# Kernel tuning notes

Measured on AMD Instinct MI355X. Metric: run time of the kernel, lower is better.

## Reference

```python
import jax, jax.numpy as jnp
import numpy as np

B, T, IN, H, L = 256, 80, 39, 256, 5


def _xavier(key, shape):
    fan_out, fan_in = shape[0], shape[1]
    std = (2.0 / (fan_in + fan_out)) ** 0.5
    return std * jax.random.normal(key, shape, dtype=jnp.float32)


def setup_inputs() -> dict:
    key = jax.random.key(0)
    ks = jax.random.split(key, 4 + 2 * L)
    x = jax.random.normal(ks[0], (B, T, IN), dtype=jnp.float32)
    # PyTorch LSTM params, gate order (i, f, g, o); biases zero per init.
    W_ih0 = _xavier(ks[1], (4 * H, IN))                       # layer 0 input weights
    W_ih_rest = jnp.stack([_xavier(ks[2 + l], (4 * H, H)) for l in range(L - 1)])  # [L-1,4H,H]
    W_hh = jnp.stack([_xavier(ks[1 + L + l], (4 * H, H)) for l in range(L)])       # [L,4H,H]
    b_ih = jnp.zeros((L, 4 * H), dtype=jnp.float32)
    b_hh = jnp.zeros((L, 4 * H), dtype=jnp.float32)
    fc_w = _xavier(ks[2 * L + 1], (1, H))
    fc_b = jnp.zeros((1,), dtype=jnp.float32)
    return {"x": x, "W_ih0": W_ih0, "W_ih_rest": W_ih_rest, "W_hh": W_hh,
            "b_ih": b_ih, "b_hh": b_hh, "fc_w": fc_w, "fc_b": fc_b}


def _lstm_layer(xs, W_ih, W_hh_l, b_ih_l, b_hh_l):
    # xs: [B,T,D]. Precompute input projection for all timesteps (one big GEMM).
    x_proj = jnp.einsum('btd,gd->btg', xs, W_ih) + b_ih_l + b_hh_l  # [B,T,4H]

    def step(carry, xp):
        h, c = carry
        gates = xp + h @ W_hh_l.T                 # [B,4H]
        i, f, g, o = jnp.split(gates, 4, axis=-1)
        c = jax.nn.sigmoid(f) * c + jax.nn.sigmoid(i) * jnp.tanh(g)
        h = jax.nn.sigmoid(o) * jnp.tanh(c)
        return (h, c), h

    b = xs.shape[0]
    h0 = jnp.zeros((b, H), dtype=xs.dtype)
    _, hs = jax.lax.scan(step, (h0, h0), jnp.swapaxes(x_proj, 0, 1))
    return jnp.swapaxes(hs, 0, 1)  # [B,T,H]


def reference(x, W_ih0, W_ih_rest, W_hh, b_ih, b_hh, fc_w, fc_b):
    h = _lstm_layer(x, W_ih0, W_hh[0], b_ih[0], b_hh[0])
    for l in range(1, L):
        h = _lstm_layer(h, W_ih_rest[l - 1], W_hh[l], b_ih[l], b_hh[l])
    out = jnp.einsum('bth,oh->bto', h, fc_w) + fc_b  # [B,T,1]
    return out[..., 0]  # [B,T]
```

## Files before the change

kernel.cpp:

```cpp
#include <hip/hip_runtime.h>

#define B_ 256
#define T_ 80
#define IN_ 39
#define H_ 256
#define G_ 1024
#define L_ 5
#define TC_ 16
#define NCH_ 5

#define XP_FLOATS   (B_ * TC_ * G_)
#define HBUF_FLOATS (B_ * T_ * H_)
#define CBUF_FLOATS (B_ * H_)
#define WG_FLOATS   (L_ * G_ * H_)
#define HX_FLOATS   (2 * 32 * 2048)
#define FLG_OFF_FLOATS (XP_FLOATS + HBUF_FLOATS + CBUF_FLOATS + WG_FLOATS + HX_FLOATS)

#define AG __HIP_MEMORY_SCOPE_AGENT

__device__ __forceinline__ float sigm(float x) { return 1.0f / (1.0f + expf(-x)); }
__device__ __forceinline__ void fma4(float4& a, float s, const float4& w) {
    a.x = fmaf(s, w.x, a.x); a.y = fmaf(s, w.y, a.y);
    a.z = fmaf(s, w.z, a.z); a.w = fmaf(s, w.w, a.w);
}
__device__ __forceinline__ void red4(float4& a) {
    a.x += __shfl_xor(a.x, 32); a.y += __shfl_xor(a.y, 32);
    a.z += __shfl_xor(a.z, 32); a.w += __shfl_xor(a.w, 32);
}

__device__ __forceinline__ void ld_mall_32B(const float* p, float4& a, float4& b) {
    asm volatile("global_load_dwordx4 %0, %2, off sc0 sc1\n\t"
                 "global_load_dwordx4 %1, %2, off offset:16 sc0 sc1\n\t"
                 "s_waitcnt vmcnt(0)"
                 : "=&v"(a), "=&v"(b) : "v"(p) : "memory");
}

extern "C" __global__ void __launch_bounds__(256)
wt_kernel(const float* __restrict__ Whh, float* __restrict__ Wg) {
    const int gid = blockIdx.x * 256 + threadIdx.x;
    const int g4 = gid & 3;
    const int j  = (gid >> 2) & 31;
    const int k  = (gid >> 7) & 255;
    const int s  = (gid >> 15) & 7;
    const int l  = gid >> 18;
    Wg[gid] = Whh[((size_t)(l * 1024 + g4 * 256 + s * 32 + j)) * 256 + k];
}

extern "C" __global__ void __launch_bounds__(256)
proj_kernel(const float* __restrict__ src, const float* __restrict__ Wih,
            const float* __restrict__ bihl, const float* __restrict__ bhhl,
            float* __restrict__ xp, int K, int t0) {
    __shared__ float As[16 * 68];
    __shared__ float Bs[16 * 68];
    const int tid = threadIdx.x;
    const int mt = blockIdx.x >> 4, nt = blockIdx.x & 15;
    const int tx = tid & 15, ty = tid >> 4;
    const int lr = tid >> 2, lc4 = (tid & 3) << 2;

    const int ar = mt * 64 + lr;
    const int ab = ar >> 4;
    const int at = t0 + (ar & 15);
    const float* arow = src + ((size_t)ab * T_ + at) * K;
    const int brow_idx = (lr & 3) * 256 + nt * 16 + (lr >> 2);
    const float* brow = Wih + (size_t)brow_idx * K;

    float acc[4][4];
    #pragma unroll
    for (int i = 0; i < 4; ++i)
        #pragma unroll
        for (int j = 0; j < 4; ++j) acc[i][j] = 0.0f;

    for (int k0 = 0; k0 < K; k0 += 16) {
        __syncthreads();
        if (K == IN_) {
            #pragma unroll
            for (int i = 0; i < 4; ++i) {
                int k = k0 + lc4 + i;
                As[(lc4 + i) * 68 + lr] = (k < IN_) ? arow[k] : 0.0f;
                Bs[(lc4 + i) * 68 + lr] = (k < IN_) ? brow[k] : 0.0f;
            }
        } else {
            float4 av = *(const float4*)(arow + k0 + lc4);
            float4 bv = *(const float4*)(brow + k0 + lc4);
            As[(lc4 + 0) * 68 + lr] = av.x;
            As[(lc4 + 1) * 68 + lr] = av.y;
            As[(lc4 + 2) * 68 + lr] = av.z;
            As[(lc4 + 3) * 68 + lr] = av.w;
            Bs[(lc4 + 0) * 68 + lr] = bv.x;
            Bs[(lc4 + 1) * 68 + lr] = bv.y;
            Bs[(lc4 + 2) * 68 + lr] = bv.z;
            Bs[(lc4 + 3) * 68 + lr] = bv.w;
        }
        __syncthreads();
        #pragma unroll
        for (int kk = 0; kk < 16; ++kk) {
            float4 a4 = *(const float4*)&As[kk * 68 + ty * 4];
            float4 b4 = *(const float4*)&Bs[kk * 68 + tx * 4];
            acc[0][0] += a4.x * b4.x; acc[0][1] += a4.x * b4.y;
            acc[0][2] += a4.x * b4.z; acc[0][3] += a4.x * b4.w;
            acc[1][0] += a4.y * b4.x; acc[1][1] += a4.y * b4.y;
            acc[1][2] += a4.y * b4.z; acc[1][3] += a4.y * b4.w;
            acc[2][0] += a4.z * b4.x; acc[2][1] += a4.z * b4.y;
            acc[2][2] += a4.z * b4.z; acc[2][3] += a4.z * b4.w;
            acc[3][0] += a4.w * b4.x; acc[3][1] += a4.w * b4.y;
            acc[3][2] += a4.w * b4.z; acc[3][3] += a4.w * b4.w;
        }
    }
    const int unit = nt * 16 + tx;
    const float bs0 = bihl[0 * 256 + unit] + bhhl[0 * 256 + unit];
    const float bs1 = bihl[1 * 256 + unit] + bhhl[1 * 256 + unit];
    const float bs2 = bihl[2 * 256 + unit] + bhhl[2 * 256 + unit];
    const float bs3 = bihl[3 * 256 + unit] + bhhl[3 * 256 + unit];
    #pragma unroll
    for (int i = 0; i < 4; ++i) {
        const int row = mt * 64 + ty * 4 + i;
        float4 o;
        o.x = acc[i][0] + bs0; o.y = acc[i][1] + bs1;
        o.z = acc[i][2] + bs2; o.w = acc[i][3] + bs3;
        *(float4*)&xp[(size_t)row * G_ + unit * 4] = o;
    }
}

extern "C" __global__ void __launch_bounds__(512, 2)
rec8_kernel(const float* __restrict__ xp, const float* __restrict__ Wg_l,
            float* __restrict__ hbuf, float* __restrict__ cbuf,
            float* __restrict__ hx, int* __restrict__ flg,
            int t0, int chkb, int first) {
    __shared__ float sH[2048];
    __shared__ float sP[8 * 32 * 36];

    const int tid = threadIdx.x;
    const int bid = blockIdx.x;
    const int grp = bid & 31;
    const int s   = bid >> 5;
    const int jj  = tid & 31;
    const int ks  = tid >> 5;
    const int w   = tid >> 6;
    const int fb  = (tid >> 5) & 7;
    const int fj  = tid & 31;
    const int bglob = grp * 8 + fb;
    const int unit  = s * 32 + fj;
    int* flg_g = flg + grp * 32;

    const float4* Wg4 = (const float4*)Wg_l + (size_t)s * 8192;
    float4 wreg[16];
    #pragma unroll
    for (int kk = 0; kk < 16; ++kk)
        wreg[kk] = Wg4[(size_t)(ks * 16 + kk) * 32 + jj];

    float creg = 0.0f;
    if (tid < 256 && !first) creg = cbuf[(size_t)bglob * H_ + unit];

    const float4* sH4 = (const float4*)sH;

    for (int tt = 0; tt < TC_; ++tt) {
        const int t = t0 + tt;

        float x0 = 0.f, x1 = 0.f, x2 = 0.f, x3 = 0.f;
        if (tid < 256) {
            const float4 xv = *(const float4*)&xp[((size_t)bglob * TC_ + tt) * G_ + unit * 4];
            x0 = xv.x; x1 = xv.y; x2 = xv.z; x3 = xv.w;
        }

        if (tt == 0) {
            if (first) {
                for (int i = tid; i < 2048; i += 512) sH[i] = 0.0f;
            } else if (tid < 256) {
                const int u = tid;
                #pragma unroll
                for (int bb = 0; bb < 8; ++bb)
                    sH[u * 8 + bb] = hbuf[((size_t)(grp * 8 + bb) * T_ + (t0 - 1)) * H_ + u];
            }
        } else {
            if (tid < 8) {
                const int tgt = chkb + tt;
                while (__hip_atomic_load(flg_g + tid, __ATOMIC_RELAXED, AG) < tgt)
                    __builtin_amdgcn_s_sleep(1);
            }
            __syncthreads();
            if (tid < 256) {
                const float* hsf = hx + (size_t)(((tt - 1) & 1) * 32 + grp) * 2048
                                      + (size_t)tid * 8;
                float4 fa, fbv;
                ld_mall_32B(hsf, fa, fbv);
                *(float4*)&sH[tid * 8] = fa;
                *(float4*)&sH[tid * 8 + 4] = fbv;
            }
        }

        __syncthreads();

        float4 a0 = {0,0,0,0}, a1 = {0,0,0,0}, a2 = {0,0,0,0}, a3 = {0,0,0,0};
        float4 a4 = {0,0,0,0}, a5 = {0,0,0,0}, a6 = {0,0,0,0}, a7 = {0,0,0,0};
        #pragma unroll
        for (int kk = 0; kk < 16; ++kk) {
            const int k = ks * 16 + kk;
            const float4 wv = wreg[kk];
            const float4 ha = sH4[k * 2];
            const float4 hb = sH4[k * 2 + 1];
            fma4(a0, ha.x, wv); fma4(a1, ha.y, wv);
            fma4(a2, ha.z, wv); fma4(a3, ha.w, wv);
            fma4(a4, hb.x, wv); fma4(a5, hb.y, wv);
            fma4(a6, hb.z, wv); fma4(a7, hb.w, wv);
        }
        red4(a0); red4(a1); red4(a2); red4(a3);
        red4(a4); red4(a5); red4(a6); red4(a7);
        if ((tid & 63) < 32) {
            float4* pp = (float4*)&sP[(w * 32 + jj) * 36];
            pp[0] = a0; pp[1] = a1; pp[2] = a2; pp[3] = a3;
            pp[4] = a4; pp[5] = a5; pp[6] = a6; pp[7] = a7;
        }
        __syncthreads();

        if (tid < 256) {
            float4 g4;
            g4.x = x0; g4.y = x1; g4.z = x2; g4.w = x3;
            #pragma unroll
            for (int w2 = 0; w2 < 8; ++w2) {
                const float4 pw = *(const float4*)&sP[(w2 * 32 + fj) * 36 + fb * 4];
                g4.x += pw.x; g4.y += pw.y; g4.z += pw.z; g4.w += pw.w;
            }
            const float I = sigm(g4.x);
            const float F = sigm(g4.y);
            const float Gt = tanhf(g4.z);
            const float O = sigm(g4.w);
            creg = F * creg + I * Gt;
            const float hval = O * tanhf(creg);
            hbuf[((size_t)bglob * T_ + t) * H_ + unit] = hval;

            if (tt < TC_ - 1) {
                const float hpart = __shfl_xor(hval, 32);
                if ((fb & 1) == 0) {
                    const unsigned long long pv =
                        ((unsigned long long)__float_as_uint(hpart) << 32)
                        | __float_as_uint(hval);
                    unsigned long long* dst = (unsigned long long*)
                        (hx + (size_t)((tt & 1) * 32 + grp) * 2048 + unit * 8 + fb);
                    __hip_atomic_store(dst, pv, __ATOMIC_RELAXED, AG);
                }
            }
        }

        if (tt < TC_ - 1) {
            asm volatile("s_waitcnt vmcnt(0)" ::: "memory");
            __syncthreads();
            if (tid == 0)
                __hip_atomic_store(flg_g + s, chkb + tt + 1, __ATOMIC_RELAXED, AG);
        }
    }

    if (tid < 256) cbuf[(size_t)bglob * H_ + unit] = creg;
}

extern "C" __global__ void __launch_bounds__(128)
fc_kernel(const float* __restrict__ hbuf, const float* __restrict__ fcw,
          const float* __restrict__ fcb, float* __restrict__ out) {
    __shared__ float wsm[256];
    const int tid = threadIdx.x;
    const int b = blockIdx.x;
    if (tid < 64) ((float4*)wsm)[tid] = ((const float4*)fcw)[tid];
    __syncthreads();
    if (tid < T_) {
        const float4* h4p = (const float4*)(hbuf + ((size_t)b * T_ + tid) * H_);
        const float4* w4p = (const float4*)wsm;
        float acc = fcb[0];
        #pragma unroll 8
        for (int k4 = 0; k4 < 64; ++k4) {
            float4 h4 = h4p[k4], w4 = w4p[k4];
            acc += h4.x * w4.x + h4.y * w4.y + h4.z * w4.z + h4.w * w4.w;
        }
        out[b * T_ + tid] = acc;
    }
}

extern "C" void kernel_launch(void* const* d_in, const int* in_sizes, int n_in,
                              void* d_out, int out_size, void* d_ws, size_t ws_size,
                              hipStream_t stream) {
    (void)in_sizes; (void)n_in; (void)out_size; (void)ws_size;
    const float* x    = (const float*)d_in[0];
    const float* Wih0 = (const float*)d_in[1];
    const float* Wihr = (const float*)d_in[2];
    const float* Whh  = (const float*)d_in[3];
    const float* bih  = (const float*)d_in[4];
    const float* bhh  = (const float*)d_in[5];
    const float* fcw  = (const float*)d_in[6];
    const float* fcb  = (const float*)d_in[7];
    float* out = (float*)d_out;
    float* ws  = (float*)d_ws;

    float* xp   = ws;
    float* hbuf = ws + XP_FLOATS;
    float* cbuf = hbuf + HBUF_FLOATS;
    float* wg   = cbuf + CBUF_FLOATS;
    float* hx   = wg + WG_FLOATS;
    int*   flg  = (int*)(ws + FLG_OFF_FLOATS);

    hipMemsetAsync(flg, 0, 32 * 32 * sizeof(int), stream);
    hipLaunchKernelGGL(wt_kernel, dim3(WG_FLOATS / 256), dim3(256), 0, stream, Whh, wg);

    for (int l = 0; l < L_; ++l) {
        const int K = (l == 0) ? IN_ : H_;
        const float* src = (l == 0) ? x : hbuf;
        const float* Wih = (l == 0) ? Wih0 : (Wihr + (size_t)(l - 1) * G_ * H_);
        const float* Wg_l = wg + (size_t)l * (G_ * H_);
        for (int ch = 0; ch < NCH_; ++ch) {
            const int t0 = ch * TC_;
            const int chkb = (l * NCH_ + ch) * (TC_ - 1);
            hipLaunchKernelGGL(proj_kernel, dim3(1024), dim3(256), 0, stream,
                               src, Wih, bih + l * G_, bhh + l * G_, xp, K, t0);
            hipLaunchKernelGGL(rec8_kernel, dim3(256), dim3(512), 0, stream,
                               xp, Wg_l, hbuf, cbuf, hx, flg, t0, chkb, ch == 0 ? 1 : 0);
        }
    }
    hipLaunchKernelGGL(fc_kernel, dim3(B_), dim3(128), 0, stream, hbuf, fcw, fcb, out);
}
```

Measured before the change: 2.541 ms.

## Split recurrent step into two batch halves with separate flags to pipeline exchange

The recurrent kernel now processes each timestep in two halves of four batch rows each. Every half has its own flag set and its own half-sized h exchange load, so one half's global handoff can overlap the other half's matvec. Per-step h outputs go into a shared-memory history buffer and are written to hbuf once at the end of the chunk instead of on every step. The cost is twice as many barriers and flag waits per step, and a larger shared-memory footprint that could reduce occupancy.

```diff
diff --git a/kernel.cpp b/kernel.cpp
--- a/kernel.cpp
+++ b/kernel.cpp
@@ -28,11 +28,12 @@
     a.z += __shfl_xor(a.z, 32); a.w += __shfl_xor(a.w, 32);
 }
 
-__device__ __forceinline__ void ld_mall_32B(const float* p, float4& a, float4& b) {
-    asm volatile("global_load_dwordx4 %0, %2, off sc0 sc1\n\t"
-                 "global_load_dwordx4 %1, %2, off offset:16 sc0 sc1\n\t"
+__device__ __forceinline__ float4 ld_mall_16B(const float* p) {
+    float4 v;
+    asm volatile("global_load_dwordx4 %0, %1, off sc0 sc1\n\t"
                  "s_waitcnt vmcnt(0)"
-                 : "=&v"(a), "=&v"(b) : "v"(p) : "memory");
+                 : "=&v"(v) : "v"(p) : "memory");
+    return v;
 }
 
 extern "C" __global__ void __launch_bounds__(256)
@@ -122,12 +123,13 @@
 }
 
 extern "C" __global__ void __launch_bounds__(512, 2)
-rec8_kernel(const float* __restrict__ xp, const float* __restrict__ Wg_l,
+rec9_kernel(const float* __restrict__ xp, const float* __restrict__ Wg_l,
             float* __restrict__ hbuf, float* __restrict__ cbuf,
             float* __restrict__ hx, int* __restrict__ flg,
             int t0, int chkb, int first) {
     __shared__ float sH[2048];
     __shared__ float sP[8 * 32 * 36];
+    __shared__ float sHist[8 * 32 * 16];
 
     const int tid = threadIdx.x;
     const int bid = blockIdx.x;
@@ -136,11 +138,10 @@
     const int jj  = tid & 31;
     const int ks  = tid >> 5;
     const int w   = tid >> 6;
-    const int fb  = (tid >> 5) & 7;
+    const int fbb = (tid >> 5) & 7;
     const int fj  = tid & 31;
-    const int bglob = grp * 8 + fb;
+    const int bglob = grp * 8 + fbb;
     const int unit  = s * 32 + fj;
-    int* flg_g = flg + grp * 32;
 
     const float4* Wg4 = (const float4*)Wg_l + (size_t)s * 8192;
     float4 wreg[16];
@@ -154,102 +155,108 @@
     const float4* sH4 = (const float4*)sH;
 
     for (int tt = 0; tt < TC_; ++tt) {
-        const int t = t0 + tt;
-
         float x0 = 0.f, x1 = 0.f, x2 = 0.f, x3 = 0.f;
         if (tid < 256) {
             const float4 xv = *(const float4*)&xp[((size_t)bglob * TC_ + tt) * G_ + unit * 4];
             x0 = xv.x; x1 = xv.y; x2 = xv.z; x3 = xv.w;
         }
 
-        if (tt == 0) {
-            if (first) {
-                for (int i = tid; i < 2048; i += 512) sH[i] = 0.0f;
-            } else if (tid < 256) {
-                const int u = tid;
+        #pragma unroll
+        for (int c = 0; c < 2; ++c) {
+            if (tt == 0) {
+                if (c == 0) {
+                    if (first) {
+                        for (int i = tid; i < 2048; i += 512) sH[i] = 0.0f;
+                    } else if (tid < 256) {
+                        #pragma unroll
+                        for (int bb = 0; bb < 8; ++bb)
+                            sH[tid * 8 + bb] =
+                                hbuf[((size_t)(grp * 8 + bb) * T_ + (t0 - 1)) * H_ + tid];
+                    }
+                }
+            } else {
+                if (tid < 8) {
+                    int* fp = flg + (grp * 2 + c) * 32 + tid;
+                    const int tgt = chkb + tt;
+                    while (__hip_atomic_load(fp, __ATOMIC_RELAXED, AG) < tgt)
+                        __builtin_amdgcn_s_sleep(1);
+                }
+            }
+            __syncthreads();
+
+            if (tt > 0 && tid < 256) {
+                const float* hsf = hx + (size_t)(((tt - 1) & 1) * 32 + grp) * 2048
+                                      + (size_t)tid * 8 + c * 4;
+                *(float4*)&sH[tid * 8 + c * 4] = ld_mall_16B(hsf);
+            }
+            __syncthreads();
+
+            float4 a0 = {0,0,0,0}, a1 = {0,0,0,0}, a2 = {0,0,0,0}, a3 = {0,0,0,0};
+            #pragma unroll
+            for (int kk = 0; kk < 16; ++kk) {
+                const int k = ks * 16 + kk;
+                const float4 wv = wreg[kk];
+                const float4 hc = sH4[k * 2 + c];
+                fma4(a0, hc.x, wv); fma4(a1, hc.y, wv);
+                fma4(a2, hc.z, wv); fma4(a3, hc.w, wv);
+            }
+            red4(a0); red4(a1); red4(a2); red4(a3);
+            if ((tid & 63) < 32) {
+                float4* pp = (float4*)&sP[(w * 32 + jj) * 36];
+                pp[0] = a0; pp[1] = a1; pp[2] = a2; pp[3] = a3;
+            }
+            __syncthreads();
+
+            if (tid < 256 && (tid >> 7) == c) {
+                const int fb2 = fbb & 3;
+                float4 g4;
+                g4.x = x0; g4.y = x1; g4.z = x2; g4.w = x3;
                 #pragma unroll
-                for (int bb = 0; bb < 8; ++bb)
-                    sH[u * 8 + bb] = hbuf[((size_t)(grp * 8 + bb) * T_ + (t0 - 1)) * H_ + u];
-            }
-        } else {
-            if (tid < 8) {
-                const int tgt = chkb + tt;
-                while (__hip_atomic_load(flg_g + tid, __ATOMIC_RELAXED, AG) < tgt)
-                    __builtin_amdgcn_s_sleep(1);
-            }
-            __syncthreads();
-            if (tid < 256) {
-                const float* hsf = hx + (size_t)(((tt - 1) & 1) * 32 + grp) * 2048
-                                      + (size_t)tid * 8;
-                float4 fa, fbv;
-                ld_mall_32B(hsf, fa, fbv);
-                *(float4*)&sH[tid * 8] = fa;
-                *(float4*)&sH[tid * 8 + 4] = fbv;
-            }
-        }
-
-        __syncthreads();
-
-        float4 a0 = {0,0,0,0}, a1 = {0,0,0,0}, a2 = {0,0,0,0}, a3 = {0,0,0,0};
-        float4 a4 = {0,0,0,0}, a5 = {0,0,0,0}, a6 = {0,0,0,0}, a7 = {0,0,0,0};
+                for (int w2 = 0; w2 < 8; ++w2) {
+                    const float4 pw = *(const float4*)&sP[(w2 * 32 + fj) * 36 + fb2 * 4];
+                    g4.x += pw.x; g4.y += pw.y; g4.z += pw.z; g4.w += pw.w;
+                }
+                const float I = sigm(g4.x);
+                const float F = sigm(g4.y);
+                const float Gt = tanhf(g4.z);
+                const float O = sigm(g4.w);
+                creg = F * creg + I * Gt;
+                const float hval = O * tanhf(creg);
+                sHist[(fbb * 32 + fj) * 16 + tt] = hval;
+
+                if (tt < TC_ - 1) {
+                    const float hpart = __shfl_xor(hval, 32);
+                    if ((fb2 & 1) == 0) {
+                        const unsigned long long pv =
+                            ((unsigned long long)__float_as_uint(hpart) << 32)
+                            | __float_as_uint(hval);
+                        unsigned long long* dst = (unsigned long long*)
+                            (hx + (size_t)((tt & 1) * 32 + grp) * 2048
+                                + unit * 8 + c * 4 + fb2);
+                        __hip_atomic_store(dst, pv, __ATOMIC_RELAXED, AG);
+                    }
+                }
+            }
+
+            if (tt < TC_ - 1) {
+                asm volatile("s_waitcnt vmcnt(0)" ::: "memory");
+                __syncthreads();
+                if (tid == 0)
+                    __hip_atomic_store(flg + (grp * 2 + c) * 32 + s, chkb + tt + 1,
+                                       __ATOMIC_RELAXED, AG);
+            } else {
+                __syncthreads();
+            }
+        }
+    }
+
+    if (tid < 256) {
         #pragma unroll
-        for (int kk = 0; kk < 16; ++kk) {
-            const int k = ks * 16 + kk;
-            const float4 wv = wreg[kk];
-            const float4 ha = sH4[k * 2];
-            const float4 hb = sH4[k * 2 + 1];
-            fma4(a0, ha.x, wv); fma4(a1, ha.y, wv);
-            fma4(a2, ha.z, wv); fma4(a3, ha.w, wv);
-            fma4(a4, hb.x, wv); fma4(a5, hb.y, wv);
-            fma4(a6, hb.z, wv); fma4(a7, hb.w, wv);
-        }
-        red4(a0); red4(a1); red4(a2); red4(a3);
-        red4(a4); red4(a5); red4(a6); red4(a7);
-        if ((tid & 63) < 32) {
-            float4* pp = (float4*)&sP[(w * 32 + jj) * 36];
-            pp[0] = a0; pp[1] = a1; pp[2] = a2; pp[3] = a3;
-            pp[4] = a4; pp[5] = a5; pp[6] = a6; pp[7] = a7;
-        }
-        __syncthreads();
-
-        if (tid < 256) {
-            float4 g4;
-            g4.x = x0; g4.y = x1; g4.z = x2; g4.w = x3;
-            #pragma unroll
-            for (int w2 = 0; w2 < 8; ++w2) {
-                const float4 pw = *(const float4*)&sP[(w2 * 32 + fj) * 36 + fb * 4];
-                g4.x += pw.x; g4.y += pw.y; g4.z += pw.z; g4.w += pw.w;
-            }
-            const float I = sigm(g4.x);
-            const float F = sigm(g4.y);
-            const float Gt = tanhf(g4.z);
-            const float O = sigm(g4.w);
-            creg = F * creg + I * Gt;
-            const float hval = O * tanhf(creg);
-            hbuf[((size_t)bglob * T_ + t) * H_ + unit] = hval;
-
-            if (tt < TC_ - 1) {
-                const float hpart = __shfl_xor(hval, 32);
-                if ((fb & 1) == 0) {
-                    const unsigned long long pv =
-                        ((unsigned long long)__float_as_uint(hpart) << 32)
-                        | __float_as_uint(hval);
-                    unsigned long long* dst = (unsigned long long*)
-                        (hx + (size_t)((tt & 1) * 32 + grp) * 2048 + unit * 8 + fb);
-                    __hip_atomic_store(dst, pv, __ATOMIC_RELAXED, AG);
-                }
-            }
-        }
-
-        if (tt < TC_ - 1) {
-            asm volatile("s_waitcnt vmcnt(0)" ::: "memory");
-            __syncthreads();
-            if (tid == 0)
-                __hip_atomic_store(flg_g + s, chkb + tt + 1, __ATOMIC_RELAXED, AG);
-        }
-    }
-
-    if (tid < 256) cbuf[(size_t)bglob * H_ + unit] = creg;
+        for (int tt = 0; tt < TC_; ++tt)
+            hbuf[((size_t)bglob * T_ + (t0 + tt)) * H_ + unit] =
+                sHist[(fbb * 32 + fj) * 16 + tt];
+        cbuf[(size_t)bglob * H_ + unit] = creg;
+    }
 }
 
 extern "C" __global__ void __launch_bounds__(128)
@@ -295,7 +302,7 @@
     float* hx   = wg + WG_FLOATS;
     int*   flg  = (int*)(ws + FLG_OFF_FLOATS);
 
-    hipMemsetAsync(flg, 0, 32 * 32 * sizeof(int), stream);
+    hipMemsetAsync(flg, 0, 64 * 32 * sizeof(int), stream);
     hipLaunchKernelGGL(wt_kernel, dim3(WG_FLOATS / 256), dim3(256), 0, stream, Whh, wg);
 
     for (int l = 0; l < L_; ++l) {
@@ -308,7 +315,7 @@
             const int chkb = (l * NCH_ + ch) * (TC_ - 1);
             hipLaunchKernelGGL(proj_kernel, dim3(1024), dim3(256), 0, stream,
                                src, Wih, bih + l * G_, bhh + l * G_, xp, K, t0);
-            hipLaunchKernelGGL(rec8_kernel, dim3(256), dim3(512), 0, stream,
+            hipLaunchKernelGGL(rec9_kernel, dim3(256), dim3(512), 0, stream,
                                xp, Wg_l, hbuf, cbuf, hx, flg, t0, chkb, ch == 0 ? 1 : 0);
         }
     }
```

After: 2.933 ms. 1.15x slower.
